# Kernel optimization log

Hardware: AMD Instinct MI355X
Metric: run time of the kernel (lower is better)

## Reference

```python
import jax, jax.numpy as jnp
import numpy as np

# ---- static problem dims (mirror the Triton kernel's constexprs) ----
NUM_SEQS = 2
LQ = 1024            # query tokens per sequence (uniform varlen instance)
HIST = 1024          # cached-prefix length per sequence
LK = LQ + HIST       # total kv length per sequence
NUM_HEADS = 32
NUM_KV_HEADS = 8
HEAD_DIM = 128
BLOCK_SIZE = 64
MAX_NUM_BLOCKS = LK // BLOCK_SIZE          # 32 logical blocks per sequence
TOTAL_BLOCKS = NUM_SEQS * MAX_NUM_BLOCKS   # physical blocks in the cache
NEG = -1e10                                # matches kernel's -10000000000.0


def setup_inputs() -> dict:
    key = jax.random.key(0)
    k1, k2, k3, k4 = jax.random.split(key, 4)
    q = jax.random.normal(k1, (NUM_SEQS * LQ, NUM_HEADS, HEAD_DIM), jnp.float32)
    k_cache = jax.random.normal(k2, (TOTAL_BLOCKS, BLOCK_SIZE, NUM_KV_HEADS, HEAD_DIM), jnp.float32)
    v_cache = jax.random.normal(k3, (TOTAL_BLOCKS, BLOCK_SIZE, NUM_KV_HEADS, HEAD_DIM), jnp.float32)
    cu_seqlens_q = (jnp.arange(NUM_SEQS + 1, dtype=jnp.int32) * LQ)
    cu_seqlens_k = (jnp.arange(NUM_SEQS + 1, dtype=jnp.int32) * LK)
    # scattered physical block layout: a random permutation -> irregular gather
    block_tables = jax.random.permutation(k4, TOTAL_BLOCKS).astype(jnp.int32).reshape(NUM_SEQS, MAX_NUM_BLOCKS)
    return dict(q=q, k_cache=k_cache, v_cache=v_cache,
                cu_seqlens_q=cu_seqlens_q, cu_seqlens_k=cu_seqlens_k,
                block_tables=block_tables)


def _paged_prefill_attention(q, k_cache, v_cache, cu_seqlens_q, cu_seqlens_k, block_tables):
    scale = 1.0 / np.sqrt(HEAD_DIM)
    seq_len_q = cu_seqlens_q[1:] - cu_seqlens_q[:-1]            # [S]
    seq_len_k = cu_seqlens_k[1:] - cu_seqlens_k[:-1]            # [S]
    history_len = seq_len_k - seq_len_q                          # [S]

    # uniform varlen instance: flat [total_q, H, D] -> [S, LQ, H, D]
    qr = q.reshape(NUM_SEQS, LQ, NUM_HEADS, HEAD_DIM)
    group = NUM_HEADS // NUM_KV_HEADS
    # [S, LQ, KVH, G, D] so head h maps to kv head h // group (kernel's kv_head_idx)
    q5 = qr.reshape(NUM_SEQS, LQ, NUM_KV_HEADS, group, HEAD_DIM) * scale

    # block-table gather: logical kv layout per sequence
    safe_tables = jnp.maximum(block_tables, 0)
    k = k_cache[safe_tables].reshape(NUM_SEQS, LK, NUM_KV_HEADS, HEAD_DIM)
    v = v_cache[safe_tables].reshape(NUM_SEQS, LK, NUM_KV_HEADS, HEAD_DIM)

    # scores [S, KVH, G, LQ, LK]
    scores = jnp.einsum('sqhgd,skhd->shgqk', q5, k)

    pos_q = jnp.arange(LQ, dtype=jnp.int32)[None, :] + history_len[:, None]   # [S, LQ] absolute positions
    pos_k = jnp.arange(LK, dtype=jnp.int32)                                   # [LK]
    valid_k = (pos_k[None, :] < seq_len_k[:, None]) & \
              jnp.repeat(block_tables >= 0, BLOCK_SIZE, axis=1)               # [S, LK]
    causal = pos_q[:, :, None] >= pos_k[None, None, :]                        # [S, LQ, LK]
    mask = causal & valid_k[:, None, :]
    scores = jnp.where(mask[:, None, None, :, :], scores, NEG)

    p = jax.nn.softmax(scores, axis=-1)  # online-softmax in kernel == exact softmax
    out = jnp.einsum('shgqk,skhd->sqhgd', p, v)
    return out.reshape(NUM_SEQS * LQ, NUM_HEADS, HEAD_DIM)


def reference(q, k_cache, v_cache, cu_seqlens_q, cu_seqlens_k, block_tables):
    return _paged_prefill_attention(q, k_cache, v_cache, cu_seqlens_q, cu_seqlens_k, block_tables)
```

## Files before the change

### kernel.cpp

```cpp
#include <hip/hip_runtime.h>
#include <hip/hip_bf16.h>

#define NS_    2
#define LQ_    1024
#define HIST_  1024
#define LK_    2048
#define NH_    32
#define NKVH_  8
#define HD_    128
#define BS_    64
#define BM_    128
#define MAXB_  32

typedef __attribute__((ext_vector_type(8))) short short8;
typedef __attribute__((ext_vector_type(4))) float f32x4;
typedef __attribute__((ext_vector_type(16))) float f32x16;
typedef __attribute__((ext_vector_type(2))) int int2v;

#define VSTR 72

static __device__ __forceinline__ unsigned short f2bf(float x) {
    __hip_bfloat16 h = __float2bfloat16(x);
    return *(unsigned short*)&h;
}

static __device__ __forceinline__ void cp16(const void* g, void* l) {
    __builtin_amdgcn_global_load_lds(
        (const __attribute__((address_space(1))) void*)g,
        (__attribute__((address_space(3))) void*)l, 16, 0, 0);
}

__global__ __launch_bounds__(256)
void prep_kv(const float* __restrict__ kc, const float* __restrict__ vc,
             const int* __restrict__ bt,
             unsigned short* __restrict__ Kb, unsigned short* __restrict__ Vb)
{
    __shared__ __align__(16) unsigned short Vt[HD_ * VSTR];
    const int tid = threadIdx.x;
    const int gid = blockIdx.x;
    const int seq = gid >> 8;
    const int kvh = (gid >> 5) & 7;
    const int blk = gid & 31;
    const int ph  = bt[seq * MAXB_ + blk];
    const size_t src = ((size_t)ph * BS_ * NKVH_ + kvh) * HD_;
    const int grp = seq * NKVH_ + kvh;
    const int t8 = tid >> 5, q32 = tid & 31;

    float4 kr[8], vr[8];
#pragma unroll
    for (int p = 0; p < 8; ++p)
        kr[p] = *(const float4*)(kc + src + (size_t)(p * 8 + t8) * (NKVH_ * HD_) + q32 * 4);
#pragma unroll
    for (int j = 0; j < 8; ++j)
        vr[j] = *(const float4*)(vc + src + (size_t)(t8 * 8 + j) * (NKVH_ * HD_) + q32 * 4);

#pragma unroll
    for (int p = 0; p < 8; ++p) {
        unsigned short u[4] = {f2bf(kr[p].x), f2bf(kr[p].y), f2bf(kr[p].z), f2bf(kr[p].w)};
        *(uint2*)(Kb + ((size_t)grp * LK_ + blk * BS_ + p * 8 + t8) * HD_ + q32 * 4) = *(const uint2*)u;
    }
#pragma unroll
    for (int w2 = 0; w2 < 4; ++w2) {
        unsigned short row[8];
#pragma unroll
        for (int j = 0; j < 8; ++j) {
            float f = (w2 == 0) ? vr[j].x : (w2 == 1) ? vr[j].y : (w2 == 2) ? vr[j].z : vr[j].w;
            row[j] = f2bf(f);
        }
        *(short8*)&Vt[(q32 * 4 + w2) * VSTR + t8 * 8] = *(const short8*)row;
    }
    __syncthreads();
#pragma unroll
    for (int u = 0; u < 4; ++u) {
        const int c  = tid + 256 * u;
        const int d  = c >> 3, ch = c & 7;
        uint4 x = *(const uint4*)&Vt[d * VSTR + ch * 8];
        *(uint4*)(Vb + ((size_t)grp * HD_ + d) * LK_ + blk * BS_ + ch * 8) = x;
    }
}

template<int MODE>
__global__ __launch_bounds__(256, 2)
void pattn(const float* __restrict__ q,
           const unsigned short* __restrict__ Kb,
           const unsigned short* __restrict__ Vb,
           const float* __restrict__ kc,
           const float* __restrict__ vc,
           const int* __restrict__ bt,
           float* __restrict__ out)
{
    __shared__ __align__(16) unsigned short SH[40960];
#define KSH(buf) (&SH[(buf) * 8192])
#define VSH(s)   (&SH[16384 + (s) * 8192])

    const int tid  = threadIdx.x;
    const int w    = tid >> 6;
    const int lane = tid & 63;
    const int m    = lane & 31;
    const int h    = lane >> 5;

    const int gid  = blockIdx.x;
    const int kvh  = gid & 7;
    const int slot = gid >> 3;
    const int seq  = slot >> 5;
    const int sub  = slot & 31;
    const int e    = sub & 1;
    const int t3   = (sub >> 1) & 7;
    const int hp   = sub >> 4;
    const int head = kvh * 4 + hp * 2 + e;
    const int t0   = (e ? (7 - t3) : t3);
    const int m0   = (seq ? (7 - t0) : t0) * BM_;
    const int r0   = m0 + w * 32;
    const int grp  = seq * NKVH_ + kvh;

    const float SC = 0.08838834764831845f * 1.4426950408889634f;
    short8 qf[8];
    {
        const size_t qbase = ((size_t)((seq * LQ_ + r0 + m) * NH_ + head)) * HD_ + h * 8;
#pragma unroll
        for (int c = 0; c < 8; ++c) {
            float4 a = *(const float4*)(q + qbase + c * 16);
            float4 b = *(const float4*)(q + qbase + c * 16 + 4);
            unsigned short u[8] = {f2bf(a.x * SC), f2bf(a.y * SC), f2bf(a.z * SC), f2bf(a.w * SC),
                                   f2bf(b.x * SC), f2bf(b.y * SC), f2bf(b.z * SC), f2bf(b.w * SC)};
            qf[c] = *(const short8*)u;
        }
    }

    f32x16 acc[4];
#pragma unroll
    for (int dt = 0; dt < 4; ++dt)
#pragma unroll
        for (int r = 0; r < 16; ++r) acc[dt][r] = 0.f;
    float lsum = 0.f;

    const int nb = (HIST_ + m0 + BM_ - 1) / BS_ + 1;
    const unsigned short* kSrc = Kb + (size_t)grp * LK_ * HD_;
    const unsigned short* vSrc = Vb + (size_t)grp * HD_ * LK_;

    auto issue = [&](int b, int kbuf, int vs) {
#pragma unroll
        for (int j = 0; j < 4; ++j) {
            const int row = w * 16 + j * 4 + (lane >> 4);
            const int c8  = (lane & 15) ^ (row & 15);
            cp16(kSrc + ((size_t)b * BS_ + row) * HD_ + c8 * 8, &KSH(kbuf)[(w * 16 + j * 4) * HD_]);
        }
#pragma unroll
        for (int j = 0; j < 4; ++j) {
            const int sr  = w * 16 + j * 4 + (lane >> 4);
            const int cc  = (lane & 15) ^ (sr & 15);
            const int dd  = 2 * sr + (cc >> 3);
            const int cht = cc & 7;
            cp16(vSrc + (size_t)dd * LK_ + b * BS_ + cht * 8, &VSH(vs)[(w * 16 + j * 4) * 128]);
        }
    };

    auto do_pv = [&](const short8* pfv, int vs) {
        __builtin_amdgcn_s_setprio(1);
#pragma unroll
        for (int ks = 0; ks < 4; ++ks) {
#pragma unroll
            for (int dt = 0; dt < 4; ++dt) {
                const int d   = dt * 32 + m;
                const int sr  = 16 * dt + (m >> 1);
                const int slt = (((d & 1) << 3) + 2 * ks + h) ^ (sr & 15);
                short8 vf = *(const short8*)&VSH(vs)[sr * 128 + slt * 8];
                acc[dt] = __builtin_amdgcn_mfma_f32_32x32x16_bf16(pfv[ks], vf, acc[dt], 0, 0, 0);
            }
        }
        __builtin_amdgcn_s_setprio(0);
    };

    if constexpr (MODE >= 1) issue(0, 0, 0);

    int vcur = 0;
    bool pvalid = false;
    int pvs = 0;
    short8 pfp[4];

    for (int b = 0; b < nb; ++b) {
        const int cur = (MODE >= 1) ? (b & 1) : 0;
        __syncthreads();
        if constexpr (MODE >= 1) {
            if (b + 1 < nb) {
                int vnx = vcur + 1; if (vnx == 3) vnx = 0;
                issue(b + 1, 1 ^ cur, vnx);
            }
        } else {
            const int ph = bt[seq * MAXB_ + b];
            const size_t src = ((size_t)ph * BS_ * NKVH_ + kvh) * HD_;
#pragma unroll
            for (int j = 0; j < 4; ++j) {
                const int row = w * 16 + j * 4 + (lane >> 4);
                const int c8  = (lane & 15) ^ (row & 15);
                float4 a = *(const float4*)(kc + src + (size_t)row * (NKVH_ * HD_) + c8 * 8);
                float4 b2 = *(const float4*)(kc + src + (size_t)row * (NKVH_ * HD_) + c8 * 8 + 4);
                unsigned short u[8] = {f2bf(a.x), f2bf(a.y), f2bf(a.z), f2bf(a.w),
                                       f2bf(b2.x), f2bf(b2.y), f2bf(b2.z), f2bf(b2.w)};
                *(short8*)&KSH(0)[row * HD_ + (lane & 15) * 8] = *(const short8*)u;
            }
#pragma unroll
            for (int j = 0; j < 4; ++j) {
                const int sr  = w * 16 + j * 4 + (lane >> 4);
                const int cc  = (lane & 15) ^ (sr & 15);
                const int dd  = 2 * sr + (cc >> 3);
                const int cht = cc & 7;
                unsigned short u[8];
#pragma unroll
                for (int i2 = 0; i2 < 8; ++i2)
                    u[i2] = f2bf(vc[src + (size_t)(cht * 8 + i2) * (NKVH_ * HD_) + dd]);
                *(short8*)&VSH(0)[sr * 128 + (lane & 15) * 8] = *(const short8*)u;
            }
            __syncthreads();
        }

        const bool active = (64 * b <= HIST_ + r0 + 31);
        f32x16 s[2];
        if (active) {
#pragma unroll
            for (int kt = 0; kt < 2; ++kt)
#pragma unroll
                for (int r = 0; r < 16; ++r) s[kt][r] = 0.f;
            __builtin_amdgcn_s_setprio(1);
#pragma unroll
            for (int c = 0; c < 8; ++c) {
#pragma unroll
                for (int kt = 0; kt < 2; ++kt) {
                    const int row  = kt * 32 + m;
                    const int slt  = (2 * c + h) ^ (row & 15);
                    short8 kf = *(const short8*)&KSH(cur)[row * HD_ + slt * 8];
                    s[kt] = __builtin_amdgcn_mfma_f32_32x32x16_bf16(kf, qf[c], s[kt], 0, 0, 0);
                }
            }
            __builtin_amdgcn_s_setprio(0);
        }

        if constexpr (MODE >= 1) {
            if (pvalid) { do_pv(pfp, pvs); pvalid = false; }
        }

        if (active) {
            if (64 * b + 63 > HIST_ + r0) {
                const int thr = HIST_ + r0 + m - 64 * b;
#pragma unroll
                for (int kt = 0; kt < 2; ++kt)
#pragma unroll
                    for (int r = 0; r < 16; ++r) {
                        const int kl = kt * 32 + (r & 3) + 8 * (r >> 2) + 4 * h;
                        if (kl > thr) s[kt][r] = -1e30f;
                    }
            }
            float ls = 0.f;
#pragma unroll
            for (int kt = 0; kt < 2; ++kt)
#pragma unroll
                for (int r = 0; r < 16; ++r) {
                    s[kt][r] = __builtin_amdgcn_exp2f(s[kt][r]);
                    ls += s[kt][r];
                }
            int wlo[8], whi[8];
#pragma unroll
            for (int u = 0; u < 8; ++u) {
                const int kt = u >> 2, rb = (u & 3) * 4;
                int a, bb;
                asm("v_cvt_pk_bf16_f32 %0, %1, %2" : "=v"(a)  : "v"(s[kt][rb]),     "v"(s[kt][rb + 1]));
                asm("v_cvt_pk_bf16_f32 %0, %1, %2" : "=v"(bb) : "v"(s[kt][rb + 2]), "v"(s[kt][rb + 3]));
                wlo[u] = a; whi[u] = bb;
            }
#pragma unroll
            for (int ks = 0; ks < 4; ++ks) {
                int2v ab = __builtin_amdgcn_permlane32_swap(wlo[2 * ks], wlo[2 * ks + 1], false, false);
                int2v cd = __builtin_amdgcn_permlane32_swap(whi[2 * ks], whi[2 * ks + 1], false, false);
                int w4[4] = { ab[0], cd[0], ab[1], cd[1] };
                pfp[ks] = *(const short8*)w4;
            }
            ls += __shfl_xor(ls, 32);
            lsum += ls;

            if constexpr (MODE >= 1) {
                pvalid = true; pvs = vcur;
            } else {
                do_pv(pfp, 0);
            }
        }
        if constexpr (MODE >= 1) { vcur = vcur + 1; if (vcur == 3) vcur = 0; }
    }
    if constexpr (MODE >= 1) {
        if (pvalid) do_pv(pfp, pvs);
    }

    {
        const float rl = 1.0f / lsum;
        float rlr[16];
#pragma unroll
        for (int r = 0; r < 16; ++r)
            rlr[r] = __shfl(rl, (r & 3) + 8 * (r >> 2) + 4 * h);
#pragma unroll
        for (int dt = 0; dt < 4; ++dt)
#pragma unroll
            for (int r = 0; r < 16; ++r) {
                const int rloc = (r & 3) + 8 * (r >> 2) + 4 * h;
                out[((size_t)((seq * LQ_ + r0 + rloc) * NH_ + head)) * HD_ + dt * 32 + m] =
                    acc[dt][r] * rlr[r];
            }
    }
#undef KSH
#undef VSH
}

extern "C" void kernel_launch(void* const* d_in, const int* in_sizes, int n_in,
                              void* d_out, int out_size, void* d_ws, size_t ws_size,
                              hipStream_t stream) {
    const float* q  = (const float*)d_in[0];
    const float* kc = (const float*)d_in[1];
    const float* vc = (const float*)d_in[2];
    const int*   bt = (const int*)d_in[5];
    float*      out = (float*)d_out;
    (void)in_sizes; (void)n_in; (void)out_size;

    const size_t kb_elems = (size_t)NS_ * NKVH_ * LK_ * HD_;
    const size_t need = kb_elems * 2 * sizeof(unsigned short);
    if (ws_size >= need) {
        unsigned short* Kb = (unsigned short*)d_ws;
        unsigned short* Vb = Kb + kb_elems;
        prep_kv<<<512, 256, 0, stream>>>(kc, vc, bt, Kb, Vb);
        pattn<1><<<512, 256, 0, stream>>>(q, Kb, Vb, kc, vc, bt, out);
    } else {
        pattn<0><<<512, 256, 0, stream>>>(q, nullptr, nullptr, kc, vc, bt, out);
    }
}
```

Baseline: 167.2 us.

## Fuse KV bf16 conversion into attention kernel with register-prefetched pipeline

Drops the separate prep_kv pass that converted and transposed the paged fp32 K/V cache into a bf16 workspace. The attention kernel now gathers fp32 K/V straight from the block table into registers one block ahead, converts to bf16, and writes them into double/triple-buffered LDS after the current block's compute. V is transposed in LDS with a new XOR swizzle. This removes a kernel launch and the workspace write and re-read. In exchange, every attention block reads fp32 K/V (twice the bytes, repeated across the many CTAs sharing each kv head), does the conversion itself, uses more registers for the prefetch, and loses the async global-to-LDS copies.

```diff
diff --git a/kernel.cpp b/kernel.cpp
--- a/kernel.cpp
+++ b/kernel.cpp
@@ -17,87 +17,28 @@
 typedef __attribute__((ext_vector_type(16))) float f32x16;
 typedef __attribute__((ext_vector_type(2))) int int2v;
 
-#define VSTR 72
-
 static __device__ __forceinline__ unsigned short f2bf(float x) {
     __hip_bfloat16 h = __float2bfloat16(x);
     return *(unsigned short*)&h;
 }
 
-static __device__ __forceinline__ void cp16(const void* g, void* l) {
-    __builtin_amdgcn_global_load_lds(
-        (const __attribute__((address_space(1))) void*)g,
-        (__attribute__((address_space(3))) void*)l, 16, 0, 0);
-}
-
-__global__ __launch_bounds__(256)
-void prep_kv(const float* __restrict__ kc, const float* __restrict__ vc,
-             const int* __restrict__ bt,
-             unsigned short* __restrict__ Kb, unsigned short* __restrict__ Vb)
-{
-    __shared__ __align__(16) unsigned short Vt[HD_ * VSTR];
-    const int tid = threadIdx.x;
-    const int gid = blockIdx.x;
-    const int seq = gid >> 8;
-    const int kvh = (gid >> 5) & 7;
-    const int blk = gid & 31;
-    const int ph  = bt[seq * MAXB_ + blk];
-    const size_t src = ((size_t)ph * BS_ * NKVH_ + kvh) * HD_;
-    const int grp = seq * NKVH_ + kvh;
-    const int t8 = tid >> 5, q32 = tid & 31;
-
-    float4 kr[8], vr[8];
-#pragma unroll
-    for (int p = 0; p < 8; ++p)
-        kr[p] = *(const float4*)(kc + src + (size_t)(p * 8 + t8) * (NKVH_ * HD_) + q32 * 4);
-#pragma unroll
-    for (int j = 0; j < 8; ++j)
-        vr[j] = *(const float4*)(vc + src + (size_t)(t8 * 8 + j) * (NKVH_ * HD_) + q32 * 4);
-
-#pragma unroll
-    for (int p = 0; p < 8; ++p) {
-        unsigned short u[4] = {f2bf(kr[p].x), f2bf(kr[p].y), f2bf(kr[p].z), f2bf(kr[p].w)};
-        *(uint2*)(Kb + ((size_t)grp * LK_ + blk * BS_ + p * 8 + t8) * HD_ + q32 * 4) = *(const uint2*)u;
-    }
-#pragma unroll
-    for (int w2 = 0; w2 < 4; ++w2) {
-        unsigned short row[8];
-#pragma unroll
-        for (int j = 0; j < 8; ++j) {
-            float f = (w2 == 0) ? vr[j].x : (w2 == 1) ? vr[j].y : (w2 == 2) ? vr[j].z : vr[j].w;
-            row[j] = f2bf(f);
-        }
-        *(short8*)&Vt[(q32 * 4 + w2) * VSTR + t8 * 8] = *(const short8*)row;
-    }
-    __syncthreads();
-#pragma unroll
-    for (int u = 0; u < 4; ++u) {
-        const int c  = tid + 256 * u;
-        const int d  = c >> 3, ch = c & 7;
-        uint4 x = *(const uint4*)&Vt[d * VSTR + ch * 8];
-        *(uint4*)(Vb + ((size_t)grp * HD_ + d) * LK_ + blk * BS_ + ch * 8) = x;
-    }
-}
-
-template<int MODE>
 __global__ __launch_bounds__(256, 2)
 void pattn(const float* __restrict__ q,
-           const unsigned short* __restrict__ Kb,
-           const unsigned short* __restrict__ Vb,
            const float* __restrict__ kc,
            const float* __restrict__ vc,
            const int* __restrict__ bt,
            float* __restrict__ out)
 {
-    __shared__ __align__(16) unsigned short SH[40960];
-#define KSH(buf) (&SH[(buf) * 8192])
-#define VSH(s)   (&SH[16384 + (s) * 8192])
+    __shared__ __align__(16) unsigned short Ksh[2][BS_ * HD_];
+    __shared__ __align__(16) unsigned short Vsh[3][64 * 128];
 
     const int tid  = threadIdx.x;
     const int w    = tid >> 6;
     const int lane = tid & 63;
     const int m    = lane & 31;
     const int h    = lane >> 5;
+    const int t8   = tid >> 5;
+    const int q32  = tid & 31;
 
     const int gid  = blockIdx.x;
     const int kvh  = gid & 7;
@@ -111,7 +52,6 @@
     const int t0   = (e ? (7 - t3) : t3);
     const int m0   = (seq ? (7 - t0) : t0) * BM_;
     const int r0   = m0 + w * 32;
-    const int grp  = seq * NKVH_ + kvh;
 
     const float SC = 0.08838834764831845f * 1.4426950408889634f;
     short8 qf[8];
@@ -135,23 +75,45 @@
     float lsum = 0.f;
 
     const int nb = (HIST_ + m0 + BM_ - 1) / BS_ + 1;
-    const unsigned short* kSrc = Kb + (size_t)grp * LK_ * HD_;
-    const unsigned short* vSrc = Vb + (size_t)grp * HD_ * LK_;
-
-    auto issue = [&](int b, int kbuf, int vs) {
+
+    float4 kr[8];
+    float4 vr[8];
+    auto loadKV = [&](int b) {
+        const int ph = bt[seq * MAXB_ + b];
+        const size_t src = ((size_t)ph * BS_ * NKVH_ + kvh) * HD_;
 #pragma unroll
         for (int j = 0; j < 4; ++j) {
             const int row = w * 16 + j * 4 + (lane >> 4);
-            const int c8  = (lane & 15) ^ (row & 15);
-            cp16(kSrc + ((size_t)b * BS_ + row) * HD_ + c8 * 8, &KSH(kbuf)[(w * 16 + j * 4) * HD_]);
-        }
+            const int cc  = (lane & 15) ^ (row & 15);
+            kr[2 * j]     = *(const float4*)(kc + src + (size_t)row * (NKVH_ * HD_) + cc * 8);
+            kr[2 * j + 1] = *(const float4*)(kc + src + (size_t)row * (NKVH_ * HD_) + cc * 8 + 4);
+        }
+#pragma unroll
+        for (int j = 0; j < 8; ++j)
+            vr[j] = *(const float4*)(vc + src + (size_t)(t8 * 8 + j) * (NKVH_ * HD_) + q32 * 4);
+    };
+    auto writeKV = [&](int kbuf, int vs) {
 #pragma unroll
         for (int j = 0; j < 4; ++j) {
-            const int sr  = w * 16 + j * 4 + (lane >> 4);
-            const int cc  = (lane & 15) ^ (sr & 15);
-            const int dd  = 2 * sr + (cc >> 3);
-            const int cht = cc & 7;
-            cp16(vSrc + (size_t)dd * LK_ + b * BS_ + cht * 8, &VSH(vs)[(w * 16 + j * 4) * 128]);
+            const int row = w * 16 + j * 4 + (lane >> 4);
+            float4 a = kr[2 * j], b2 = kr[2 * j + 1];
+            unsigned short u[8] = {f2bf(a.x), f2bf(a.y), f2bf(a.z), f2bf(a.w),
+                                   f2bf(b2.x), f2bf(b2.y), f2bf(b2.z), f2bf(b2.w)};
+            *(short8*)&Ksh[kbuf][row * HD_ + (lane & 15) * 8] = *(const short8*)u;
+        }
+#pragma unroll
+        for (int w2 = 0; w2 < 4; ++w2) {
+            const int sr = q32 * 2 + (w2 >> 1);
+            const int jj = (w2 & 1) * 8 + t8;
+            const int s  = jj ^ (q32 & 7);
+            unsigned short u[8];
+#pragma unroll
+            for (int k2 = 0; k2 < 8; ++k2) {
+                float f = (w2 == 0) ? vr[k2].x : (w2 == 1) ? vr[k2].y
+                        : (w2 == 2) ? vr[k2].z : vr[k2].w;
+                u[k2] = f2bf(f);
+            }
+            *(short8*)&Vsh[vs][sr * 128 + s * 8] = *(const short8*)u;
         }
     };
 
@@ -161,17 +123,17 @@
         for (int ks = 0; ks < 4; ++ks) {
 #pragma unroll
             for (int dt = 0; dt < 4; ++dt) {
-                const int d   = dt * 32 + m;
                 const int sr  = 16 * dt + (m >> 1);
-                const int slt = (((d & 1) << 3) + 2 * ks + h) ^ (sr & 15);
-                short8 vf = *(const short8*)&VSH(vs)[sr * 128 + slt * 8];
+                const int slt = (((m & 1) << 3) + 2 * ks + h) ^ ((m >> 2) & 7);
+                short8 vf = *(const short8*)&Vsh[vs][sr * 128 + slt * 8];
                 acc[dt] = __builtin_amdgcn_mfma_f32_32x32x16_bf16(pfv[ks], vf, acc[dt], 0, 0, 0);
             }
         }
         __builtin_amdgcn_s_setprio(0);
     };
 
-    if constexpr (MODE >= 1) issue(0, 0, 0);
+    loadKV(0);
+    writeKV(0, 0);
 
     int vcur = 0;
     bool pvalid = false;
@@ -179,40 +141,10 @@
     short8 pfp[4];
 
     for (int b = 0; b < nb; ++b) {
-        const int cur = (MODE >= 1) ? (b & 1) : 0;
+        const int cur = b & 1;
         __syncthreads();
-        if constexpr (MODE >= 1) {
-            if (b + 1 < nb) {
-                int vnx = vcur + 1; if (vnx == 3) vnx = 0;
-                issue(b + 1, 1 ^ cur, vnx);
-            }
-        } else {
-            const int ph = bt[seq * MAXB_ + b];
-            const size_t src = ((size_t)ph * BS_ * NKVH_ + kvh) * HD_;
-#pragma unroll
-            for (int j = 0; j < 4; ++j) {
-                const int row = w * 16 + j * 4 + (lane >> 4);
-                const int c8  = (lane & 15) ^ (row & 15);
-                float4 a = *(const float4*)(kc + src + (size_t)row * (NKVH_ * HD_) + c8 * 8);
-                float4 b2 = *(const float4*)(kc + src + (size_t)row * (NKVH_ * HD_) + c8 * 8 + 4);
-                unsigned short u[8] = {f2bf(a.x), f2bf(a.y), f2bf(a.z), f2bf(a.w),
-                                       f2bf(b2.x), f2bf(b2.y), f2bf(b2.z), f2bf(b2.w)};
-                *(short8*)&KSH(0)[row * HD_ + (lane & 15) * 8] = *(const short8*)u;
-            }
-#pragma unroll
-            for (int j = 0; j < 4; ++j) {
-                const int sr  = w * 16 + j * 4 + (lane >> 4);
-                const int cc  = (lane & 15) ^ (sr & 15);
-                const int dd  = 2 * sr + (cc >> 3);
-                const int cht = cc & 7;
-                unsigned short u[8];
-#pragma unroll
-                for (int i2 = 0; i2 < 8; ++i2)
-                    u[i2] = f2bf(vc[src + (size_t)(cht * 8 + i2) * (NKVH_ * HD_) + dd]);
-                *(short8*)&VSH(0)[sr * 128 + (lane & 15) * 8] = *(const short8*)u;
-            }
-            __syncthreads();
-        }
+        const bool more = (b + 1 < nb);
+        if (more) loadKV(b + 1);
 
         const bool active = (64 * b <= HIST_ + r0 + 31);
         f32x16 s[2];
@@ -226,18 +158,16 @@
             for (int c = 0; c < 8; ++c) {
 #pragma unroll
                 for (int kt = 0; kt < 2; ++kt) {
-                    const int row  = kt * 32 + m;
-                    const int slt  = (2 * c + h) ^ (row & 15);
-                    short8 kf = *(const short8*)&KSH(cur)[row * HD_ + slt * 8];
+                    const int row = kt * 32 + m;
+                    const int slt = (2 * c + h) ^ (row & 15);
+                    short8 kf = *(const short8*)&Ksh[cur][row * HD_ + slt * 8];
                     s[kt] = __builtin_amdgcn_mfma_f32_32x32x16_bf16(kf, qf[c], s[kt], 0, 0, 0);
                 }
             }
             __builtin_amdgcn_s_setprio(0);
         }
 
-        if constexpr (MODE >= 1) {
-            if (pvalid) { do_pv(pfp, pvs); pvalid = false; }
-        }
+        if (pvalid) { do_pv(pfp, pvs); pvalid = false; }
 
         if (active) {
             if (64 * b + 63 > HIST_ + r0) {
@@ -276,18 +206,16 @@
             }
             ls += __shfl_xor(ls, 32);
             lsum += ls;
-
-            if constexpr (MODE >= 1) {
-                pvalid = true; pvs = vcur;
-            } else {
-                do_pv(pfp, 0);
-            }
-        }
-        if constexpr (MODE >= 1) { vcur = vcur + 1; if (vcur == 3) vcur = 0; }
+            pvalid = true; pvs = vcur;
+        }
+
+        if (more) {
+            int vnx = vcur + 1; if (vnx == 3) vnx = 0;
+            writeKV(1 ^ cur, vnx);
+            vcur = vnx;
+        }
     }
-    if constexpr (MODE >= 1) {
-        if (pvalid) do_pv(pfp, pvs);
-    }
+    if (pvalid) do_pv(pfp, pvs);
 
     {
         const float rl = 1.0f / lsum;
@@ -304,8 +232,6 @@
                     acc[dt][r] * rlr[r];
             }
     }
-#undef KSH
-#undef VSH
 }
 
 extern "C" void kernel_launch(void* const* d_in, const int* in_sizes, int n_in,
@@ -316,16 +242,7 @@
     const float* vc = (const float*)d_in[2];
     const int*   bt = (const int*)d_in[5];
     float*      out = (float*)d_out;
-    (void)in_sizes; (void)n_in; (void)out_size;
-
-    const size_t kb_elems = (size_t)NS_ * NKVH_ * LK_ * HD_;
-    const size_t need = kb_elems * 2 * sizeof(unsigned short);
-    if (ws_size >= need) {
-        unsigned short* Kb = (unsigned short*)d_ws;
-        unsigned short* Vb = Kb + kb_elems;
-        prep_kv<<<512, 256, 0, stream>>>(kc, vc, bt, Kb, Vb);
-        pattn<1><<<512, 256, 0, stream>>>(q, Kb, Vb, kc, vc, bt, out);
-    } else {
-        pattn<0><<<512, 256, 0, stream>>>(q, nullptr, nullptr, kc, vc, bt, out);
-    }
+    (void)in_sizes; (void)n_in; (void)out_size; (void)d_ws; (void)ws_size;
+
+    pattn<<<512, 256, 0, stream>>>(q, kc, vc, bt, out);
 }
```

Measured after the change: 233.0 us. 39.4% more time.
